# Optimization experiments

Measured on AMD Instinct MI355X. Metric: run time of the kernel, lower is better.

The kernel has to match this reference:

```python
import jax, jax.numpy as jnp
import numpy as np

# Module constants (from init_kwargs)
TRUNC = (32, 32, 32)
OUT_SIZE = (32, 32, 32)
HOMOMORPHIC = False


def dct2_ortho_mat(N):
    """Orthonormal DCT-II matrix C of shape [N, N]; y = C @ x along an axis.
    IDCT (DCT-III ortho) is C.T since C is orthogonal."""
    n = jnp.arange(N, dtype=jnp.float32)          # sample index
    k = n[:, None]                                 # frequency index
    C = jnp.cos(jnp.pi * (2.0 * n + 1.0) * k / (2.0 * N))
    scale = jnp.where(k == 0, jnp.sqrt(1.0 / N), jnp.sqrt(2.0 / N))
    return (C * scale).astype(jnp.float32)


def _transform3d(x, Cd, Ch, Cw):
    # Apply separable 1D transforms along D, H, W axes of [B, C, D, H, W].
    x = jnp.einsum('kd,bcdhw->bckhw', Cd, x)
    x = jnp.einsum('kh,bcdhw->bcdkw', Ch, x)
    x = jnp.einsum('kw,bcdhw->bcdhk', Cw, x)
    return x


def setup_inputs() -> dict:
    key = jax.random.key(0)
    x = jax.random.normal(key, (4, 32, 64, 64, 64), dtype=jnp.float32)
    return {"x": x}


def reference(x) -> jnp.ndarray:
    B, C, D, H, W = x.shape
    if HOMOMORPHIC:
        x = jnp.log(x + 1e-6)

    # 3D DCT-II (ortho) along D, H, W
    Cd, Ch, Cw = dct2_ortho_mat(D), dct2_ortho_mat(H), dct2_ortho_mat(W)
    x_dct = _transform3d(x, Cd, Ch, Cw)

    # Crop low frequencies to `truncation`, zero-pad up to `output_size`
    t0, t1, t2 = TRUNC
    o0, o1, o2 = OUT_SIZE
    x_crop = x_dct[:, :, :t0, :t1, :t2]
    x_pad = jnp.pad(x_crop, ((0, 0), (0, 0), (0, o0 - t0), (0, o1 - t1), (0, o2 - t2)))

    # 3D IDCT (DCT-III ortho) = transpose of the ortho DCT-II matrix
    Id, Ih, Iw = dct2_ortho_mat(o0).T, dct2_ortho_mat(o1).T, dct2_ortho_mat(o2).T
    out = _transform3d(x_pad, Id, Ih, Iw)

    if HOMOMORPHIC:
        out = jnp.exp(out)
    return out
```

## Files before the change

### kernel.cpp

```cpp
#include <hip/hip_runtime.h>
#include <math.h>
#include <stdint.h>


#define PI_F 3.14159265358979323846f

typedef __attribute__((ext_vector_type(4))) float f32x4;
typedef __attribute__((ext_vector_type(8))) short bf16x8;

union U16x8 { uint4 q; bf16x8 v; };

__device__ __forceinline__ unsigned short bf16r(float x) {
    union { float f; uint32_t u; } c; c.f = x;
    uint32_t r = (c.u + 0x7FFFu + ((c.u >> 16) & 1u)) >> 16;
    return (unsigned short)r;
}
__device__ __forceinline__ uint32_t bfpack(float a, float b) {
    return (uint32_t)bf16r(a) | ((uint32_t)bf16r(b) << 16);
}

__device__ __forceinline__ float Aelem(int i, int d) {
    const float s1 = sqrtf(1.0f / 32.0f), s2 = sqrtf(2.0f / 32.0f);
    const float t1 = sqrtf(1.0f / 64.0f), t2 = sqrtf(2.0f / 64.0f);
    float acc = 0.f;
    for (int k = 0; k < 32; ++k) {
        int n1 = ((2 * i + 1) * k) & 127;
        int n2 = ((2 * d + 1) * k) & 255;
        float c1 = cosf((float)n1 * (PI_F / 64.0f));
        float c2 = cosf((float)n2 * (PI_F / 128.0f));
        acc += ((k == 0) ? s1 : s2) * ((k == 0) ? t1 : t2) * c1 * c2;
    }
    return acc;
}

__global__ __launch_bounds__(256) void build_tables(float* __restrict__ At,
                                                    unsigned short* __restrict__ F) {
    int e = blockIdx.x * 256 + threadIdx.x;
    if (e < 2048) {
        int d = e >> 5, i = e & 31;
        At[e] = Aelem(i, d);
    } else if (e < 4096) {
        int f = e - 2048;
        int jj = f & 7, lane = (f >> 3) & 63, tk = f >> 9;
        int tt = tk >> 1, kt = tk & 1;
        int row = tt * 16 + (lane & 15);
        int col = kt * 32 + ((lane >> 4) << 3) + jj;
        F[f] = bf16r(Aelem(row, col));
    }
}

__global__ __launch_bounds__(256, 3) void k_hw(const float* __restrict__ x,
                                               const unsigned short* __restrict__ F,
                                               unsigned short* __restrict__ w1b) {
    __shared__ unsigned short Ut[4][2048];

    const int t = threadIdx.x;
    const int wv = t >> 6, ln = t & 63;
    const int lm = ln & 15, lg = ln >> 4;
    const size_t slab = (size_t)blockIdx.x * 4 + wv;

    const float* xs = x + slab * 4096;
    uint4 raw[16];
    #pragma unroll
    for (int mt = 0; mt < 4; ++mt)
        #pragma unroll
        for (int kt = 0; kt < 2; ++kt) {
            const uint4* p = (const uint4*)(xs + (mt * 16 + lm) * 64 + kt * 32 + (lg << 3));
            raw[(mt * 2 + kt) * 2 + 0] = p[0];
            raw[(mt * 2 + kt) * 2 + 1] = p[1];
        }

    bf16x8 Ff[2][2];
    {
        const uint4* fp = (const uint4*)F;
        #pragma unroll
        for (int tt = 0; tt < 2; ++tt)
            #pragma unroll
            for (int kt = 0; kt < 2; ++kt) {
                U16x8 u; u.q = fp[(tt * 2 + kt) * 64 + ln];
                Ff[tt][kt] = u.v;
            }
    }

    f32x4 accu[4][2];
    #pragma unroll
    for (int mt = 0; mt < 4; ++mt)
        #pragma unroll
        for (int nt = 0; nt < 2; ++nt)
            accu[mt][nt] = (f32x4){0.f, 0.f, 0.f, 0.f};

    #pragma unroll
    for (int mt = 0; mt < 4; ++mt) {
        #pragma unroll
        for (int kt = 0; kt < 2; ++kt) {
            const float* f0 = (const float*)&raw[(mt * 2 + kt) * 2];
            bf16x8 xf;
            #pragma unroll
            for (int e = 0; e < 8; ++e) xf[e] = (short)bf16r(f0[e]);
            #pragma unroll
            for (int nt = 0; nt < 2; ++nt)
                accu[mt][nt] = __builtin_amdgcn_mfma_f32_16x16x32_bf16(
                    xf, Ff[nt][kt], accu[mt][nt], 0, 0, 0);
        }
    }

    unsigned short* ut = Ut[wv];
    #pragma unroll
    for (int mt = 0; mt < 4; ++mt)
        #pragma unroll
        for (int nt = 0; nt < 2; ++nt) {
            int lo = nt * 16 + lm;
            int h0 = mt * 16 + (lg << 2);
            uint32_t w0 = bfpack(accu[mt][nt][0], accu[mt][nt][1]);
            uint32_t w1v = bfpack(accu[mt][nt][2], accu[mt][nt][3]);
            uint32_t byte = (uint32_t)(lo * 128 + 2 * h0);
            byte ^= (uint32_t)((lo & 7) << 4);
            *(uint2*)((char*)ut + byte) = make_uint2(w0, w1v);
        }
    __builtin_amdgcn_wave_barrier();

    f32x4 acco[2][2];
    #pragma unroll
    for (int mt = 0; mt < 2; ++mt)
        #pragma unroll
        for (int nt = 0; nt < 2; ++nt)
            acco[mt][nt] = (f32x4){0.f, 0.f, 0.f, 0.f};

    #pragma unroll
    for (int mt = 0; mt < 2; ++mt) {
        #pragma unroll
        for (int kt = 0; kt < 2; ++kt) {
            int lo = mt * 16 + lm;
            uint32_t byte = (uint32_t)(lo * 128 + kt * 64 + (lg << 4));
            byte ^= (uint32_t)((lo & 7) << 4);
            bf16x8 uf = *(const bf16x8*)((const char*)ut + byte);
            #pragma unroll
            for (int nt = 0; nt < 2; ++nt)
                acco[mt][nt] = __builtin_amdgcn_mfma_f32_16x16x32_bf16(
                    uf, Ff[nt][kt], acco[mt][nt], 0, 0, 0);
        }
    }

    #pragma unroll
    for (int mt = 0; mt < 2; ++mt)
        #pragma unroll
        for (int nt = 0; nt < 2; ++nt) {
            uint32_t u0 = bfpack(acco[mt][nt][0], acco[mt][nt][1]);
            uint32_t u1 = bfpack(acco[mt][nt][2], acco[mt][nt][3]);
            int j  = nt * 16 + lm;
            int l0 = mt * 16 + (lg << 2);
            *(uint2*)(w1b + slab * 1024 + j * 32 + l0) = make_uint2(u0, u1);
        }
}

__global__ __launch_bounds__(256, 4) void k_d(const unsigned short* __restrict__ w1b,
                                              const float* __restrict__ At,
                                              float* __restrict__ out) {
    const int t = threadIdx.x;
    const int bc = blockIdx.x >> 3;
    const int ks = (blockIdx.x >> 1) & 3;
    const int pq = blockIdx.x & 1;
    const int p0 = pq * 512 + t * 2;
    const unsigned short* src = w1b + (size_t)bc * 65536 + p0;
    float acc0[8], acc1[8];
    #pragma unroll
    for (int k = 0; k < 8; ++k) { acc0[k] = 0.f; acc1[k] = 0.f; }
    #pragma unroll 8
    for (int d = 0; d < 64; ++d) {
        uint32_t u = *(const uint32_t*)(src + d * 1024);
        float v0 = __uint_as_float(u << 16);
        float v1 = __uint_as_float(u & 0xFFFF0000u);
        const float* arow = At + d * 32 + ks * 8;
        #pragma unroll
        for (int k = 0; k < 8; ++k) {
            float a = arow[k];
            acc0[k] += a * v0;
            acc1[k] += a * v1;
        }
    }
    float* dst = out + (size_t)bc * 32768 + (size_t)ks * 8192 + p0;
    #pragma unroll
    for (int k = 0; k < 8; ++k)
        *(float2*)(dst + k * 1024) = make_float2(acc0[k], acc1[k]);
}

extern "C" void kernel_launch(void* const* d_in, const int* in_sizes, int n_in,
                              void* d_out, int out_size, void* d_ws, size_t ws_size,
                              hipStream_t stream) {
    const float* x = (const float*)d_in[0];
    float* out = (float*)d_out;

    float* At           = (float*)d_ws;
    unsigned short* F   = (unsigned short*)((char*)d_ws + 8192);
    unsigned short* w1b = (unsigned short*)((char*)d_ws + 16384);

    build_tables<<<16, 256, 0, stream>>>(At, F);
    k_hw<<<2048, 256, 0, stream>>>(x, F, w1b);
    k_d<<<1024, 256, 0, stream>>>(w1b, At, out);
}
```

Measured before the change: 49.86 us.

## Reorder k_hw loads into two halves and remap k_d to one column per thread

```diff
diff --git a/kernel.cpp b/kernel.cpp
--- a/kernel.cpp
+++ b/kernel.cpp
@@ -49,7 +49,7 @@
     }
 }
 
-__global__ __launch_bounds__(256, 3) void k_hw(const float* __restrict__ x,
+__global__ __launch_bounds__(256, 4) void k_hw(const float* __restrict__ x,
                                                const unsigned short* __restrict__ F,
                                                unsigned short* __restrict__ w1b) {
     __shared__ unsigned short Ut[4][2048];
@@ -59,17 +59,6 @@
     const int lm = ln & 15, lg = ln >> 4;
     const size_t slab = (size_t)blockIdx.x * 4 + wv;
 
-    const float* xs = x + slab * 4096;
-    uint4 raw[16];
-    #pragma unroll
-    for (int mt = 0; mt < 4; ++mt)
-        #pragma unroll
-        for (int kt = 0; kt < 2; ++kt) {
-            const uint4* p = (const uint4*)(xs + (mt * 16 + lm) * 64 + kt * 32 + (lg << 3));
-            raw[(mt * 2 + kt) * 2 + 0] = p[0];
-            raw[(mt * 2 + kt) * 2 + 1] = p[1];
-        }
-
     bf16x8 Ff[2][2];
     {
         const uint4* fp = (const uint4*)F;
@@ -82,6 +71,25 @@
             }
     }
 
+    const float* xs = x + slab * 4096;
+    uint4 rawA[8], rawB[8];
+    #pragma unroll
+    for (int mt = 0; mt < 2; ++mt)
+        #pragma unroll
+        for (int kt = 0; kt < 2; ++kt) {
+            const uint4* p = (const uint4*)(xs + (mt * 16 + lm) * 64 + kt * 32 + (lg << 3));
+            rawA[(mt * 2 + kt) * 2 + 0] = p[0];
+            rawA[(mt * 2 + kt) * 2 + 1] = p[1];
+        }
+    #pragma unroll
+    for (int mt = 2; mt < 4; ++mt)
+        #pragma unroll
+        for (int kt = 0; kt < 2; ++kt) {
+            const uint4* p = (const uint4*)(xs + (mt * 16 + lm) * 64 + kt * 32 + (lg << 3));
+            rawB[((mt - 2) * 2 + kt) * 2 + 0] = p[0];
+            rawB[((mt - 2) * 2 + kt) * 2 + 1] = p[1];
+        }
+
     f32x4 accu[4][2];
     #pragma unroll
     for (int mt = 0; mt < 4; ++mt)
@@ -90,10 +98,10 @@
             accu[mt][nt] = (f32x4){0.f, 0.f, 0.f, 0.f};
 
     #pragma unroll
-    for (int mt = 0; mt < 4; ++mt) {
-        #pragma unroll
-        for (int kt = 0; kt < 2; ++kt) {
-            const float* f0 = (const float*)&raw[(mt * 2 + kt) * 2];
+    for (int mt = 0; mt < 2; ++mt)
+        #pragma unroll
+        for (int kt = 0; kt < 2; ++kt) {
+            const float* f0 = (const float*)&rawA[(mt * 2 + kt) * 2];
             bf16x8 xf;
             #pragma unroll
             for (int e = 0; e < 8; ++e) xf[e] = (short)bf16r(f0[e]);
@@ -102,7 +110,19 @@
                 accu[mt][nt] = __builtin_amdgcn_mfma_f32_16x16x32_bf16(
                     xf, Ff[nt][kt], accu[mt][nt], 0, 0, 0);
         }
-    }
+    #pragma unroll
+    for (int mt = 2; mt < 4; ++mt)
+        #pragma unroll
+        for (int kt = 0; kt < 2; ++kt) {
+            const float* f0 = (const float*)&rawB[((mt - 2) * 2 + kt) * 2];
+            bf16x8 xf;
+            #pragma unroll
+            for (int e = 0; e < 8; ++e) xf[e] = (short)bf16r(f0[e]);
+            #pragma unroll
+            for (int nt = 0; nt < 2; ++nt)
+                accu[mt][nt] = __builtin_amdgcn_mfma_f32_16x16x32_bf16(
+                    xf, Ff[nt][kt], accu[mt][nt], 0, 0, 0);
+        }
 
     unsigned short* ut = Ut[wv];
     #pragma unroll
@@ -153,35 +173,29 @@
         }
 }
 
-__global__ __launch_bounds__(256, 4) void k_d(const unsigned short* __restrict__ w1b,
-                                              const float* __restrict__ At,
-                                              float* __restrict__ out) {
+__global__ __launch_bounds__(256) void k_d(const unsigned short* __restrict__ w1b,
+                                           const float* __restrict__ At,
+                                           float* __restrict__ out) {
     const int t = threadIdx.x;
     const int bc = blockIdx.x >> 3;
-    const int ks = (blockIdx.x >> 1) & 3;
-    const int pq = blockIdx.x & 1;
-    const int p0 = pq * 512 + t * 2;
-    const unsigned short* src = w1b + (size_t)bc * 65536 + p0;
-    float acc0[8], acc1[8];
-    #pragma unroll
-    for (int k = 0; k < 8; ++k) { acc0[k] = 0.f; acc1[k] = 0.f; }
+    const int kh = (blockIdx.x >> 2) & 1;
+    const int q  = blockIdx.x & 3;
+    const int p  = q * 256 + t;
+    const unsigned short* src = w1b + (size_t)bc * 65536 + p;
+    float acc[16];
+    #pragma unroll
+    for (int k = 0; k < 16; ++k) acc[k] = 0.f;
     #pragma unroll 8
     for (int d = 0; d < 64; ++d) {
-        uint32_t u = *(const uint32_t*)(src + d * 1024);
-        float v0 = __uint_as_float(u << 16);
-        float v1 = __uint_as_float(u & 0xFFFF0000u);
-        const float* arow = At + d * 32 + ks * 8;
-        #pragma unroll
-        for (int k = 0; k < 8; ++k) {
-            float a = arow[k];
-            acc0[k] += a * v0;
-            acc1[k] += a * v1;
-        }
-    }
-    float* dst = out + (size_t)bc * 32768 + (size_t)ks * 8192 + p0;
-    #pragma unroll
-    for (int k = 0; k < 8; ++k)
-        *(float2*)(dst + k * 1024) = make_float2(acc0[k], acc1[k]);
+        uint32_t u = (uint32_t)src[d * 1024];
+        float v = __uint_as_float(u << 16);
+        const float* arow = At + d * 32 + kh * 16;
+        #pragma unroll
+        for (int k = 0; k < 16; ++k) acc[k] += arow[k] * v;
+    }
+    float* dst = out + (size_t)bc * 32768 + (size_t)kh * 16384 + p;
+    #pragma unroll
+    for (int k = 0; k < 16; ++k) dst[k * 1024] = acc[k];
 }
 
 extern "C" void kernel_launch(void* const* d_in, const int* in_sizes, int n_in,
```

New measurement: 47.07 us. 5.6% less time.
